# Kernel optimization log

Measured on AMD Instinct MI355X. Metric: run time of the kernel, lower is better.

## Reference

```python
import jax, jax.numpy as jnp
import numpy as np


def _feature_map(x):
    # elu(x) + 1, the canonical positive feature map for linear attention
    return jax.nn.elu(x) + 1.0


def setup_inputs() -> dict:
    key = jax.random.key(0)
    kq, kk, kv = jax.random.split(key, 3)
    B, T, H, D, M = 2, 2048, 8, 64, 64
    q = jax.random.normal(kq, (B, T, H, D), dtype=jnp.float32)
    k = jax.random.normal(kk, (B, T, H, D), dtype=jnp.float32)
    v = jax.random.normal(kv, (B, T, H, M), dtype=jnp.float32)
    return {"q": q, "k": k, "v": v}


def reference(q, k, v):
    # q,k: [B,T,H,D]; v: [B,T,H,M]
    qf = _feature_map(q)
    kf = _feature_map(k)
    # running sum of keys over time (causal)
    k_sum = jnp.cumsum(kf, axis=1)                      # [B,T,H,D]
    z = 1.0 / jnp.einsum('bthd,bthd->bth', qf, k_sum)   # [B,T,H]
    # outer products k_i v_i^T; NOTE: original torch code cumsums over dim=-2
    # (the D axis of the [B,T,H,D,M] tensor), reproduced faithfully here.
    kv = jnp.einsum('bthd,bthm->bthdm', kf, v)           # [B,T,H,D,M]
    kv_sum = jnp.cumsum(kv, axis=-2)                     # cumsum over D, per source
    out = jnp.einsum('bthd,bthdm,bth->bthm', qf, kv_sum, z)
    return out
```

## Files before the change

kernel.cpp:

```cpp
#include <hip/hip_runtime.h>

#define BB 2
#define TT 2048
#define HH 8
#define DD 64
#define CC 256
#define TC (TT / CC)
#define STRIDE (HH * DD)
#define NBH (BB * HH)

__device__ __forceinline__ float feat(float x) {
    return x > 0.f ? x + 1.f : __expf(x);
}


__global__ void __launch_bounds__(64)
chunk_sums_kernel(const float* __restrict__ k, float* __restrict__ ws) {
    const int idx  = blockIdx.x;
    const int c    = idx & (CC - 1);
    const int h    = (idx >> 8) & (HH - 1);
    const int b    = idx >> 11;
    const int lane = threadIdx.x;
    const int g    = lane & 15;
    const int seg  = lane >> 4;

    const size_t off0 = (((size_t)b * TT + c * TC + seg) * HH + h) * DD + g * 4;
    const float4 k0 = *(const float4*)(k + off0);
    const float4 k1 = *(const float4*)(k + off0 + (size_t)4 * STRIDE);

    float4 s;
    s.x = feat(k0.x) + feat(k1.x);
    s.y = feat(k0.y) + feat(k1.y);
    s.z = feat(k0.z) + feat(k1.z);
    s.w = feat(k0.w) + feat(k1.w);

    s.x += __shfl_xor(s.x, 16, 64); s.y += __shfl_xor(s.y, 16, 64);
    s.z += __shfl_xor(s.z, 16, 64); s.w += __shfl_xor(s.w, 16, 64);
    s.x += __shfl_xor(s.x, 32, 64); s.y += __shfl_xor(s.y, 32, 64);
    s.z += __shfl_xor(s.z, 32, 64); s.w += __shfl_xor(s.w, 32, 64);

    if (seg == 0)
        *(float4*)(ws + (size_t)idx * DD + g * 4) = s;
}

__global__ void __launch_bounds__(64)
linattn_kernel(const float* __restrict__ q, const float* __restrict__ k,
               const float* __restrict__ v, const float* __restrict__ ws,
               float* __restrict__ out) {
    const int idx  = blockIdx.x;
    const int c    = idx & (CC - 1);
    const int h    = (idx >> 8) & (HH - 1);
    const int b    = idx >> 11;
    const int lane = threadIdx.x;
    const int g    = lane & 15;
    const int seg  = lane >> 4;

    const size_t off0 = (((size_t)b * TT + c * TC + seg) * HH + h) * DD + g * 4;
    const size_t off1 = off0 + (size_t)4 * STRIDE;

    float4 kf0 = *(const float4*)(k + off0);
    float4 kf1 = *(const float4*)(k + off1);
    float4 qf0 = *(const float4*)(q + off0);
    float4 qf1 = *(const float4*)(q + off1);
    const float4 vv0 = *(const float4*)(v + off0);
    const float4 vv1 = *(const float4*)(v + off1);

    const float* wsg = ws + (size_t)(idx - c) * DD + g * 4;
    float4 carry = make_float4(0.f, 0.f, 0.f, 0.f);
    for (int cp = seg; cp < c; cp += 4) {
        const float4 t = *(const float4*)(wsg + (size_t)cp * DD);
        carry.x += t.x; carry.y += t.y; carry.z += t.z; carry.w += t.w;
    }
    carry.x += __shfl_xor(carry.x, 16, 64); carry.y += __shfl_xor(carry.y, 16, 64);
    carry.z += __shfl_xor(carry.z, 16, 64); carry.w += __shfl_xor(carry.w, 16, 64);
    carry.x += __shfl_xor(carry.x, 32, 64); carry.y += __shfl_xor(carry.y, 32, 64);
    carry.z += __shfl_xor(carry.z, 32, 64); carry.w += __shfl_xor(carry.w, 32, 64);

    kf0.x = feat(kf0.x); kf0.y = feat(kf0.y); kf0.z = feat(kf0.z); kf0.w = feat(kf0.w);
    kf1.x = feat(kf1.x); kf1.y = feat(kf1.y); kf1.z = feat(kf1.z); kf1.w = feat(kf1.w);
    qf0.x = feat(qf0.x); qf0.y = feat(qf0.y); qf0.z = feat(qf0.z); qf0.w = feat(qf0.w);
    qf1.x = feat(qf1.x); qf1.y = feat(qf1.y); qf1.z = feat(qf1.z); qf1.w = feat(qf1.w);

    float4 i0 = kf0, i1 = kf1;
    {
        float u;
        u = __shfl_up(i0.x, 16, 64); if (seg >= 1) i0.x += u;
        u = __shfl_up(i0.y, 16, 64); if (seg >= 1) i0.y += u;
        u = __shfl_up(i0.z, 16, 64); if (seg >= 1) i0.z += u;
        u = __shfl_up(i0.w, 16, 64); if (seg >= 1) i0.w += u;
        u = __shfl_up(i1.x, 16, 64); if (seg >= 1) i1.x += u;
        u = __shfl_up(i1.y, 16, 64); if (seg >= 1) i1.y += u;
        u = __shfl_up(i1.z, 16, 64); if (seg >= 1) i1.z += u;
        u = __shfl_up(i1.w, 16, 64); if (seg >= 1) i1.w += u;
        u = __shfl_up(i0.x, 32, 64); if (seg >= 2) i0.x += u;
        u = __shfl_up(i0.y, 32, 64); if (seg >= 2) i0.y += u;
        u = __shfl_up(i0.z, 32, 64); if (seg >= 2) i0.z += u;
        u = __shfl_up(i0.w, 32, 64); if (seg >= 2) i0.w += u;
        u = __shfl_up(i1.x, 32, 64); if (seg >= 2) i1.x += u;
        u = __shfl_up(i1.y, 32, 64); if (seg >= 2) i1.y += u;
        u = __shfl_up(i1.z, 32, 64); if (seg >= 2) i1.z += u;
        u = __shfl_up(i1.w, 32, 64); if (seg >= 2) i1.w += u;
    }
    float4 S0;
    S0.x = __shfl(i0.x, 48 + g, 64);
    S0.y = __shfl(i0.y, 48 + g, 64);
    S0.z = __shfl(i0.z, 48 + g, 64);
    S0.w = __shfl(i0.w, 48 + g, 64);

    float4 run0, run1;
    run0.x = carry.x + i0.x; run0.y = carry.y + i0.y;
    run0.z = carry.z + i0.z; run0.w = carry.w + i0.w;
    run1.x = carry.x + S0.x + i1.x; run1.y = carry.y + S0.y + i1.y;
    run1.z = carry.z + S0.z + i1.z; run1.w = carry.w + S0.w + i1.w;

    float4 p0, p1;
    p0.x = kf0.x; p0.y = p0.x + kf0.y; p0.z = p0.y + kf0.z; p0.w = p0.z + kf0.w;
    p1.x = kf1.x; p1.y = p1.x + kf1.y; p1.z = p1.y + kf1.z; p1.w = p1.z + kf1.w;
    float c0 = p0.w, c1 = p1.w;
    #pragma unroll
    for (int o = 1; o <= 8; o <<= 1) {
        float u0 = __shfl_up(c0, o, 16);
        float u1 = __shfl_up(c1, o, 16);
        if (g >= o) { c0 += u0; c1 += u1; }
    }
    const float e0 = c0 - p0.w;
    const float e1 = c1 - p1.w;

    const float sq0 = qf0.x + qf0.y + qf0.z + qf0.w;
    const float sq1 = qf1.x + qf1.y + qf1.z + qf1.w;
    float s1_0 = qf0.x * p0.x + qf0.y * p0.y + qf0.z * p0.z + qf0.w * p0.w + e0 * sq0;
    float s2_0 = qf0.x * run0.x + qf0.y * run0.y + qf0.z * run0.z + qf0.w * run0.w;
    float s1_1 = qf1.x * p1.x + qf1.y * p1.y + qf1.z * p1.z + qf1.w * p1.w + e1 * sq1;
    float s2_1 = qf1.x * run1.x + qf1.y * run1.y + qf1.z * run1.z + qf1.w * run1.w;
    #pragma unroll
    for (int o = 1; o <= 8; o <<= 1) {
        s1_0 += __shfl_xor(s1_0, o, 64);
        s2_0 += __shfl_xor(s2_0, o, 64);
        s1_1 += __shfl_xor(s1_1, o, 64);
        s2_1 += __shfl_xor(s2_1, o, 64);
    }

    const float r0 = s1_0 * __builtin_amdgcn_rcpf(s2_0);
    const float r1 = s1_1 * __builtin_amdgcn_rcpf(s2_1);
    float4 o0, o1;
    o0.x = vv0.x * r0; o0.y = vv0.y * r0; o0.z = vv0.z * r0; o0.w = vv0.w * r0;
    o1.x = vv1.x * r1; o1.y = vv1.y * r1; o1.z = vv1.z * r1; o1.w = vv1.w * r1;
    *(float4*)(out + off0) = o0;
    *(float4*)(out + off1) = o1;
}

extern "C" void kernel_launch(void* const* d_in, const int* in_sizes, int n_in,
                              void* d_out, int out_size, void* d_ws, size_t ws_size,
                              hipStream_t stream) {
    const float* q = (const float*)d_in[0];
    const float* k = (const float*)d_in[1];
    const float* v = (const float*)d_in[2];
    float* out = (float*)d_out;
    float* ws  = (float*)d_ws;

    const int nblk = BB * HH * CC;
    chunk_sums_kernel<<<nblk, 64, 0, stream>>>(k, ws);
    linattn_kernel<<<nblk, 64, 0, stream>>>(q, k, v, ws, out);
}
```

Measured before the change: 92.62 us.

## Fuse chunk-sum and attention kernels into one cooperative grid-synced kernel

```diff
diff --git a/kernel.cpp b/kernel.cpp
--- a/kernel.cpp
+++ b/kernel.cpp
@@ -1,4 +1,7 @@
 #include <hip/hip_runtime.h>
+#include <hip/hip_cooperative_groups.h>
+
+namespace cg = cooperative_groups;
 
 #define BB 2
 #define TT 2048
@@ -7,53 +10,37 @@
 #define CC 256
 #define TC (TT / CC)
 #define STRIDE (HH * DD)
-#define NBH (BB * HH)
+#define NWAVE (BB * HH * CC)
+#define GS_OFF ((size_t)NWAVE * DD)
 
 __device__ __forceinline__ float feat(float x) {
     return x > 0.f ? x + 1.f : __expf(x);
 }
 
+__device__ __forceinline__ void feat4(float4& a) {
+    a.x = feat(a.x); a.y = feat(a.y); a.z = feat(a.z); a.w = feat(a.w);
+}
 
-__global__ void __launch_bounds__(64)
-chunk_sums_kernel(const float* __restrict__ k, float* __restrict__ ws) {
-    const int idx  = blockIdx.x;
-    const int c    = idx & (CC - 1);
-    const int h    = (idx >> 8) & (HH - 1);
-    const int b    = idx >> 11;
-    const int lane = threadIdx.x;
+__device__ __forceinline__ void xorred4(float4& a) {
+    a.x += __shfl_xor(a.x, 16, 64); a.y += __shfl_xor(a.y, 16, 64);
+    a.z += __shfl_xor(a.z, 16, 64); a.w += __shfl_xor(a.w, 16, 64);
+    a.x += __shfl_xor(a.x, 32, 64); a.y += __shfl_xor(a.y, 32, 64);
+    a.z += __shfl_xor(a.z, 32, 64); a.w += __shfl_xor(a.w, 32, 64);
+}
+
+__global__ void __launch_bounds__(256, 4)
+fused_kernel(const float* __restrict__ q, const float* __restrict__ k,
+             const float* __restrict__ v, float* __restrict__ out) {
+    const int W    = blockIdx.x * 4 + (threadIdx.x >> 6);
+    const int lane = threadIdx.x & 63;
+    const int c    = W & (CC - 1);
+    const int h    = (W >> 8) & (HH - 1);
+    const int b    = W >> 11;
     const int g    = lane & 15;
     const int seg  = lane >> 4;
 
-    const size_t off0 = (((size_t)b * TT + c * TC + seg) * HH + h) * DD + g * 4;
-    const float4 k0 = *(const float4*)(k + off0);
-    const float4 k1 = *(const float4*)(k + off0 + (size_t)4 * STRIDE);
-
-    float4 s;
-    s.x = feat(k0.x) + feat(k1.x);
-    s.y = feat(k0.y) + feat(k1.y);
-    s.z = feat(k0.z) + feat(k1.z);
-    s.w = feat(k0.w) + feat(k1.w);
-
-    s.x += __shfl_xor(s.x, 16, 64); s.y += __shfl_xor(s.y, 16, 64);
-    s.z += __shfl_xor(s.z, 16, 64); s.w += __shfl_xor(s.w, 16, 64);
-    s.x += __shfl_xor(s.x, 32, 64); s.y += __shfl_xor(s.y, 32, 64);
-    s.z += __shfl_xor(s.z, 32, 64); s.w += __shfl_xor(s.w, 32, 64);
-
-    if (seg == 0)
-        *(float4*)(ws + (size_t)idx * DD + g * 4) = s;
-}
-
-__global__ void __launch_bounds__(64)
-linattn_kernel(const float* __restrict__ q, const float* __restrict__ k,
-               const float* __restrict__ v, const float* __restrict__ ws,
-               float* __restrict__ out) {
-    const int idx  = blockIdx.x;
-    const int c    = idx & (CC - 1);
-    const int h    = (idx >> 8) & (HH - 1);
-    const int b    = idx >> 11;
-    const int lane = threadIdx.x;
-    const int g    = lane & 15;
-    const int seg  = lane >> 4;
+    float* chunkS = out;
+    float* groupS = out + GS_OFF;
 
     const size_t off0 = (((size_t)b * TT + c * TC + seg) * HH + h) * DD + g * 4;
     const size_t off1 = off0 + (size_t)4 * STRIDE;
@@ -65,21 +52,48 @@
     const float4 vv0 = *(const float4*)(v + off0);
     const float4 vv1 = *(const float4*)(v + off1);
 
-    const float* wsg = ws + (size_t)(idx - c) * DD + g * 4;
+    feat4(kf0); feat4(kf1); feat4(qf0); feat4(qf1);
+
+    float4 s;
+    s.x = kf0.x + kf1.x; s.y = kf0.y + kf1.y;
+    s.z = kf0.z + kf1.z; s.w = kf0.w + kf1.w;
+    xorred4(s);
+    if (seg == 0)
+        *(float4*)(chunkS + (size_t)W * DD + g * 4) = s;
+
+    cg::this_grid().sync();
+
+    if (W < 256) {
+        const int bh2 = W >> 4, g16 = W & 15;
+        const float* cs = chunkS + ((size_t)bh2 * CC + g16 * 16) * DD + g * 4;
+        float4 t = make_float4(0.f, 0.f, 0.f, 0.f);
+        #pragma unroll
+        for (int i = 0; i < 4; ++i) {
+            const float4 a = *(const float4*)(cs + (size_t)(seg + 4 * i) * DD);
+            t.x += a.x; t.y += a.y; t.z += a.z; t.w += a.w;
+        }
+        xorred4(t);
+        if (seg == 0)
+            *(float4*)(groupS + (size_t)W * DD + g * 4) = t;
+    }
+
+    cg::this_grid().sync();
+
+    const int bh = W >> 8;
     float4 carry = make_float4(0.f, 0.f, 0.f, 0.f);
-    for (int cp = seg; cp < c; cp += 4) {
-        const float4 t = *(const float4*)(wsg + (size_t)cp * DD);
+    const int ng = c >> 4;
+    const float* gsb = groupS + ((size_t)bh * 16) * DD + g * 4;
+    for (int gp = seg; gp < ng; gp += 4) {
+        const float4 t = *(const float4*)(gsb + (size_t)gp * DD);
         carry.x += t.x; carry.y += t.y; carry.z += t.z; carry.w += t.w;
     }
-    carry.x += __shfl_xor(carry.x, 16, 64); carry.y += __shfl_xor(carry.y, 16, 64);
-    carry.z += __shfl_xor(carry.z, 16, 64); carry.w += __shfl_xor(carry.w, 16, 64);
-    carry.x += __shfl_xor(carry.x, 32, 64); carry.y += __shfl_xor(carry.y, 32, 64);
-    carry.z += __shfl_xor(carry.z, 32, 64); carry.w += __shfl_xor(carry.w, 32, 64);
-
-    kf0.x = feat(kf0.x); kf0.y = feat(kf0.y); kf0.z = feat(kf0.z); kf0.w = feat(kf0.w);
-    kf1.x = feat(kf1.x); kf1.y = feat(kf1.y); kf1.z = feat(kf1.z); kf1.w = feat(kf1.w);
-    qf0.x = feat(qf0.x); qf0.y = feat(qf0.y); qf0.z = feat(qf0.z); qf0.w = feat(qf0.w);
-    qf1.x = feat(qf1.x); qf1.y = feat(qf1.y); qf1.z = feat(qf1.z); qf1.w = feat(qf1.w);
+    const int nc = c & 15;
+    const float* csb = chunkS + ((size_t)bh * CC + (c & ~15)) * DD + g * 4;
+    for (int cp = seg; cp < nc; cp += 4) {
+        const float4 t = *(const float4*)(csb + (size_t)cp * DD);
+        carry.x += t.x; carry.y += t.y; carry.z += t.z; carry.w += t.w;
+    }
+    xorred4(carry);
 
     float4 i0 = kf0, i1 = kf1;
     {
@@ -145,6 +159,9 @@
     float4 o0, o1;
     o0.x = vv0.x * r0; o0.y = vv0.y * r0; o0.z = vv0.z * r0; o0.w = vv0.w * r0;
     o1.x = vv1.x * r1; o1.y = vv1.y * r1; o1.z = vv1.z * r1; o1.w = vv1.w * r1;
+
+    cg::this_grid().sync();
+
     *(float4*)(out + off0) = o0;
     *(float4*)(out + off1) = o1;
 }
@@ -156,9 +173,9 @@
     const float* k = (const float*)d_in[1];
     const float* v = (const float*)d_in[2];
     float* out = (float*)d_out;
-    float* ws  = (float*)d_ws;
+    (void)d_ws; (void)ws_size;
 
-    const int nblk = BB * HH * CC;
-    chunk_sums_kernel<<<nblk, 64, 0, stream>>>(k, ws);
-    linattn_kernel<<<nblk, 64, 0, stream>>>(q, k, v, ws, out);
+    void* args[] = {(void*)&q, (void*)&k, (void*)&v, (void*)&out};
+    hipLaunchCooperativeKernel((const void*)fused_kernel,
+                               dim3(NWAVE / 4), dim3(256), args, 0, stream);
 }
```

After: 365.2 us. 294% more time.

## Use two-level hierarchical prefix sums for chunk carries

Applied to the files above, without the earlier changes.

```diff
diff --git a/kernel.cpp b/kernel.cpp
--- a/kernel.cpp
+++ b/kernel.cpp
@@ -8,39 +8,56 @@
 #define TC (TT / CC)
 #define STRIDE (HH * DD)
 #define NBH (BB * HH)
+#define NG 16
+#define GSZ 16
+#define GS_OFF ((size_t)NBH * CC * DD)
 
 __device__ __forceinline__ float feat(float x) {
     return x > 0.f ? x + 1.f : __expf(x);
 }
 
+__device__ __forceinline__ void xorred4(float4& a) {
+    a.x += __shfl_xor(a.x, 16, 64); a.y += __shfl_xor(a.y, 16, 64);
+    a.z += __shfl_xor(a.z, 16, 64); a.w += __shfl_xor(a.w, 16, 64);
+    a.x += __shfl_xor(a.x, 32, 64); a.y += __shfl_xor(a.y, 32, 64);
+    a.z += __shfl_xor(a.z, 32, 64); a.w += __shfl_xor(a.w, 32, 64);
+}
+
 
 __global__ void __launch_bounds__(64)
-chunk_sums_kernel(const float* __restrict__ k, float* __restrict__ ws) {
-    const int idx  = blockIdx.x;
-    const int c    = idx & (CC - 1);
-    const int h    = (idx >> 8) & (HH - 1);
-    const int b    = idx >> 11;
+group_sums_kernel(const float* __restrict__ k, float* __restrict__ ws) {
+    const int W    = blockIdx.x;
+    const int g16  = W & (NG - 1);
+    const int bh   = W >> 4;
     const int lane = threadIdx.x;
     const int g    = lane & 15;
     const int seg  = lane >> 4;
 
-    const size_t off0 = (((size_t)b * TT + c * TC + seg) * HH + h) * DD + g * 4;
-    const float4 k0 = *(const float4*)(k + off0);
-    const float4 k1 = *(const float4*)(k + off0 + (size_t)4 * STRIDE);
+    float* chunkS = ws;
+    float* groupS = ws + GS_OFF;
 
-    float4 s;
-    s.x = feat(k0.x) + feat(k1.x);
-    s.y = feat(k0.y) + feat(k1.y);
-    s.z = feat(k0.z) + feat(k1.z);
-    s.w = feat(k0.w) + feat(k1.w);
+    const size_t base = (size_t)(bh >> 3) * TT * STRIDE
+                      + (size_t)(bh & 7) * DD + g * 4;
 
-    s.x += __shfl_xor(s.x, 16, 64); s.y += __shfl_xor(s.y, 16, 64);
-    s.z += __shfl_xor(s.z, 16, 64); s.w += __shfl_xor(s.w, 16, 64);
-    s.x += __shfl_xor(s.x, 32, 64); s.y += __shfl_xor(s.y, 32, 64);
-    s.z += __shfl_xor(s.z, 32, 64); s.w += __shfl_xor(s.w, 32, 64);
-
+    float4 gtot = make_float4(0.f, 0.f, 0.f, 0.f);
+    #pragma unroll
+    for (int i = 0; i < GSZ; ++i) {
+        const int c = g16 * GSZ + i;
+        const size_t o0 = base + (size_t)(c * TC + seg) * STRIDE;
+        const float4 a = *(const float4*)(k + o0);
+        const float4 b = *(const float4*)(k + o0 + (size_t)4 * STRIDE);
+        float4 s;
+        s.x = feat(a.x) + feat(b.x);
+        s.y = feat(a.y) + feat(b.y);
+        s.z = feat(a.z) + feat(b.z);
+        s.w = feat(a.w) + feat(b.w);
+        xorred4(s);
+        if (seg == 0)
+            *(float4*)(chunkS + ((size_t)bh * CC + c) * DD + g * 4) = s;
+        gtot.x += s.x; gtot.y += s.y; gtot.z += s.z; gtot.w += s.w;
+    }
     if (seg == 0)
-        *(float4*)(ws + (size_t)idx * DD + g * 4) = s;
+        *(float4*)(groupS + ((size_t)bh * NG + g16) * DD + g * 4) = gtot;
 }
 
 __global__ void __launch_bounds__(64)
@@ -51,6 +68,7 @@
     const int c    = idx & (CC - 1);
     const int h    = (idx >> 8) & (HH - 1);
     const int b    = idx >> 11;
+    const int bh   = idx >> 8;
     const int lane = threadIdx.x;
     const int g    = lane & 15;
     const int seg  = lane >> 4;
@@ -65,16 +83,22 @@
     const float4 vv0 = *(const float4*)(v + off0);
     const float4 vv1 = *(const float4*)(v + off1);
 
-    const float* wsg = ws + (size_t)(idx - c) * DD + g * 4;
+    const float* chunkS = ws;
+    const float* groupS = ws + GS_OFF;
     float4 carry = make_float4(0.f, 0.f, 0.f, 0.f);
-    for (int cp = seg; cp < c; cp += 4) {
-        const float4 t = *(const float4*)(wsg + (size_t)cp * DD);
+    const int ng = c >> 4;
+    const float* gsb = groupS + ((size_t)bh * NG) * DD + g * 4;
+    for (int gp = seg; gp < ng; gp += 4) {
+        const float4 t = *(const float4*)(gsb + (size_t)gp * DD);
         carry.x += t.x; carry.y += t.y; carry.z += t.z; carry.w += t.w;
     }
-    carry.x += __shfl_xor(carry.x, 16, 64); carry.y += __shfl_xor(carry.y, 16, 64);
-    carry.z += __shfl_xor(carry.z, 16, 64); carry.w += __shfl_xor(carry.w, 16, 64);
-    carry.x += __shfl_xor(carry.x, 32, 64); carry.y += __shfl_xor(carry.y, 32, 64);
-    carry.z += __shfl_xor(carry.z, 32, 64); carry.w += __shfl_xor(carry.w, 32, 64);
+    const int nc = c & 15;
+    const float* csb = chunkS + ((size_t)bh * CC + (c & ~15)) * DD + g * 4;
+    for (int cp = seg; cp < nc; cp += 4) {
+        const float4 t = *(const float4*)(csb + (size_t)cp * DD);
+        carry.x += t.x; carry.y += t.y; carry.z += t.z; carry.w += t.w;
+    }
+    xorred4(carry);
 
     kf0.x = feat(kf0.x); kf0.y = feat(kf0.y); kf0.z = feat(kf0.z); kf0.w = feat(kf0.w);
     kf1.x = feat(kf1.x); kf1.y = feat(kf1.y); kf1.z = feat(kf1.z); kf1.w = feat(kf1.w);
@@ -158,7 +182,6 @@
     float* out = (float*)d_out;
     float* ws  = (float*)d_ws;
 
-    const int nblk = BB * HH * CC;
-    chunk_sums_kernel<<<nblk, 64, 0, stream>>>(k, ws);
-    linattn_kernel<<<nblk, 64, 0, stream>>>(q, k, v, ws, out);
+    group_sums_kernel<<<NBH * NG, 64, 0, stream>>>(k, ws);
+    linattn_kernel<<<BB * HH * CC, 64, 0, stream>>>(q, k, v, ws, out);
 }
```

New measurement: 90.41 us. 2.4% less time.

## Compute exclusive chunk prefix sums in scan kernel instead of per-block carry loops

Applied to the files above, without the earlier changes.

```diff
diff --git a/kernel.cpp b/kernel.cpp
--- a/kernel.cpp
+++ b/kernel.cpp
@@ -8,39 +8,73 @@
 #define TC (TT / CC)
 #define STRIDE (HH * DD)
 #define NBH (BB * HH)
+#define CPW (CC / 16)
 
 __device__ __forceinline__ float feat(float x) {
     return x > 0.f ? x + 1.f : __expf(x);
 }
 
+__device__ __forceinline__ void feat4(float4& a) {
+    a.x = feat(a.x); a.y = feat(a.y); a.z = feat(a.z); a.w = feat(a.w);
+}
 
-__global__ void __launch_bounds__(64)
-chunk_sums_kernel(const float* __restrict__ k, float* __restrict__ ws) {
-    const int idx  = blockIdx.x;
-    const int c    = idx & (CC - 1);
-    const int h    = (idx >> 8) & (HH - 1);
-    const int b    = idx >> 11;
-    const int lane = threadIdx.x;
+__device__ __forceinline__ void xorred4(float4& a) {
+    a.x += __shfl_xor(a.x, 16, 64); a.y += __shfl_xor(a.y, 16, 64);
+    a.z += __shfl_xor(a.z, 16, 64); a.w += __shfl_xor(a.w, 16, 64);
+    a.x += __shfl_xor(a.x, 32, 64); a.y += __shfl_xor(a.y, 32, 64);
+    a.z += __shfl_xor(a.z, 32, 64); a.w += __shfl_xor(a.w, 32, 64);
+}
+
+
+__global__ void __launch_bounds__(1024)
+scan_kernel(const float* __restrict__ k, float* __restrict__ ws) {
+    const int bh   = blockIdx.x;
+    const int w    = threadIdx.x >> 6;
+    const int lane = threadIdx.x & 63;
     const int g    = lane & 15;
     const int seg  = lane >> 4;
 
-    const size_t off0 = (((size_t)b * TT + c * TC + seg) * HH + h) * DD + g * 4;
-    const float4 k0 = *(const float4*)(k + off0);
-    const float4 k1 = *(const float4*)(k + off0 + (size_t)4 * STRIDE);
+    const int b = bh >> 3, h = bh & 7;
+    const size_t base = (((size_t)b * TT + w * CPW * TC + seg) * HH + h) * DD + g * 4;
 
-    float4 s;
-    s.x = feat(k0.x) + feat(k1.x);
-    s.y = feat(k0.y) + feat(k1.y);
-    s.z = feat(k0.z) + feat(k1.z);
-    s.w = feat(k0.w) + feat(k1.w);
+    float4 excl[CPW];
+    float4 run = make_float4(0.f, 0.f, 0.f, 0.f);
+    #pragma unroll 4
+    for (int i = 0; i < CPW; ++i) {
+        const size_t o0 = base + (size_t)(i * TC) * STRIDE;
+        float4 a = *(const float4*)(k + o0);
+        float4 c = *(const float4*)(k + o0 + (size_t)4 * STRIDE);
+        float4 s;
+        s.x = feat(a.x) + feat(c.x);
+        s.y = feat(a.y) + feat(c.y);
+        s.z = feat(a.z) + feat(c.z);
+        s.w = feat(a.w) + feat(c.w);
+        xorred4(s);
+        excl[i] = run;
+        run.x += s.x; run.y += s.y; run.z += s.z; run.w += s.w;
+    }
 
-    s.x += __shfl_xor(s.x, 16, 64); s.y += __shfl_xor(s.y, 16, 64);
-    s.z += __shfl_xor(s.z, 16, 64); s.w += __shfl_xor(s.w, 16, 64);
-    s.x += __shfl_xor(s.x, 32, 64); s.y += __shfl_xor(s.y, 32, 64);
-    s.z += __shfl_xor(s.z, 32, 64); s.w += __shfl_xor(s.w, 32, 64);
+    __shared__ float tot[16][DD];
+    if (seg == 0)
+        *(float4*)(&tot[w][g * 4]) = run;
+    __syncthreads();
 
-    if (seg == 0)
-        *(float4*)(ws + (size_t)idx * DD + g * 4) = s;
+    float4 carry = make_float4(0.f, 0.f, 0.f, 0.f);
+    for (int w2 = 0; w2 < w; ++w2) {
+        const float4 t = *(const float4*)(&tot[w2][g * 4]);
+        carry.x += t.x; carry.y += t.y; carry.z += t.z; carry.w += t.w;
+    }
+
+    if (seg == 0) {
+        float* wsb = ws + ((size_t)bh * CC + w * CPW) * DD + g * 4;
+        #pragma unroll
+        for (int i = 0; i < CPW; ++i) {
+            float4 e;
+            e.x = excl[i].x + carry.x; e.y = excl[i].y + carry.y;
+            e.z = excl[i].z + carry.z; e.w = excl[i].w + carry.w;
+            *(float4*)(wsb + (size_t)i * DD) = e;
+        }
+    }
 }
 
 __global__ void __launch_bounds__(64)
@@ -64,22 +98,9 @@
     float4 qf1 = *(const float4*)(q + off1);
     const float4 vv0 = *(const float4*)(v + off0);
     const float4 vv1 = *(const float4*)(v + off1);
+    const float4 carry = *(const float4*)(ws + (size_t)idx * DD + g * 4);
 
-    const float* wsg = ws + (size_t)(idx - c) * DD + g * 4;
-    float4 carry = make_float4(0.f, 0.f, 0.f, 0.f);
-    for (int cp = seg; cp < c; cp += 4) {
-        const float4 t = *(const float4*)(wsg + (size_t)cp * DD);
-        carry.x += t.x; carry.y += t.y; carry.z += t.z; carry.w += t.w;
-    }
-    carry.x += __shfl_xor(carry.x, 16, 64); carry.y += __shfl_xor(carry.y, 16, 64);
-    carry.z += __shfl_xor(carry.z, 16, 64); carry.w += __shfl_xor(carry.w, 16, 64);
-    carry.x += __shfl_xor(carry.x, 32, 64); carry.y += __shfl_xor(carry.y, 32, 64);
-    carry.z += __shfl_xor(carry.z, 32, 64); carry.w += __shfl_xor(carry.w, 32, 64);
-
-    kf0.x = feat(kf0.x); kf0.y = feat(kf0.y); kf0.z = feat(kf0.z); kf0.w = feat(kf0.w);
-    kf1.x = feat(kf1.x); kf1.y = feat(kf1.y); kf1.z = feat(kf1.z); kf1.w = feat(kf1.w);
-    qf0.x = feat(qf0.x); qf0.y = feat(qf0.y); qf0.z = feat(qf0.z); qf0.w = feat(qf0.w);
-    qf1.x = feat(qf1.x); qf1.y = feat(qf1.y); qf1.z = feat(qf1.z); qf1.w = feat(qf1.w);
+    feat4(kf0); feat4(kf1); feat4(qf0); feat4(qf1);
 
     float4 i0 = kf0, i1 = kf1;
     {
@@ -158,7 +179,6 @@
     float* out = (float*)d_out;
     float* ws  = (float*)d_ws;
 
-    const int nblk = BB * HH * CC;
-    chunk_sums_kernel<<<nblk, 64, 0, stream>>>(k, ws);
-    linattn_kernel<<<nblk, 64, 0, stream>>>(q, k, v, ws, out);
+    scan_kernel<<<NBH, 1024, 0, stream>>>(k, ws);
+    linattn_kernel<<<BB * HH * CC, 64, 0, stream>>>(q, k, v, ws, out);
 }
```

Result: no change. 94.32 us (+1.8%).
